# Optimization experiments

Measured on AMD Instinct MI355X. Metric: run time of the kernel, lower is better.

## Reference

```python
import jax, jax.numpy as jnp
import numpy as np

H = 128
N_ATOMS = 20000
N_BONDS = 60000
BATCH = 8


def _linear_params(key, fan_in, fan_out, bias=True):
    kw, kb = jax.random.split(key)
    lim = 1.0 / np.sqrt(fan_in)
    W = jax.random.uniform(kw, (fan_in, fan_out), jnp.float32, -lim, lim)
    if bias:
        b = jax.random.uniform(kb, (fan_out,), jnp.float32, -lim, lim)
        return W, b
    return W


def setup_inputs() -> dict:
    key = jax.random.key(0)
    ks = jax.random.split(key, 12)
    h = jax.random.normal(ks[0], (BATCH, N_ATOMS, H), jnp.float32)
    x = jax.random.normal(ks[1], (BATCH, N_ATOMS, 3), jnp.float32)
    bond_indices = jax.random.randint(ks[2], (N_BONDS, 2), 0, N_ATOMS, jnp.int64)
    Wm1, bm1 = _linear_params(ks[3], 2 * H + 1, H)
    Wm2, bm2 = _linear_params(ks[4], H, H)
    Wn1, bn1 = _linear_params(ks[5], 2 * H, H)
    Wn2, bn2 = _linear_params(ks[6], H, H)
    Wc1, bc1 = _linear_params(ks[7], H, H)
    # xavier_uniform gain=0.001 for final coord layer [1, H] in torch -> [H, 1] here
    lim = 0.001 * np.sqrt(6.0 / (H + 1))
    Wc2 = jax.random.uniform(ks[8], (H, 1), jnp.float32, -lim, lim)
    return dict(h=h, x=x, bond_indices=bond_indices,
                Wm1=Wm1, bm1=bm1, Wm2=Wm2, bm2=bm2,
                Wn1=Wn1, bn1=bn1, Wn2=Wn2, bn2=bn2,
                Wc1=Wc1, bc1=bc1, Wc2=Wc2)


def reference(h, x, bond_indices, Wm1, bm1, Wm2, bm2, Wn1, bn1, Wn2, bn2, Wc1, bc1, Wc2):
    silu = jax.nn.silu
    n_atoms = h.shape[1]
    src = bond_indices[:, 0]
    dst = bond_indices[:, 1]

    h_src = h[:, src, :]            # [B, E, H]
    h_dst = h[:, dst, :]
    coord_diff = x[:, dst, :] - x[:, src, :]   # [B, E, 3]
    dist = jnp.linalg.norm(coord_diff, axis=-1, keepdims=True)  # [B, E, 1]

    mi = jnp.concatenate([h_src, h_dst, dist], axis=-1)  # [B, E, 2H+1]
    messages = silu(silu(mi @ Wm1 + bm1) @ Wm2 + bm2)    # [B, E, H]

    aggregated = jnp.zeros_like(h).at[:, dst, :].add(messages).at[:, src, :].add(messages)

    h_in = jnp.concatenate([h, aggregated], axis=-1)     # [B, N, 2H]
    h_out = h + (silu(h_in @ Wn1 + bn1) @ Wn2 + bn2)

    coord_weights = silu(messages @ Wc1 + bc1) @ Wc2     # [B, E, 1]
    coord_diff_norm = coord_diff / (dist + 1e-8)
    upd = coord_diff_norm * coord_weights                # [B, E, 3]
    coord_update = jnp.zeros_like(x).at[:, dst, :].add(upd).at[:, src, :].add(-upd)

    ones = jnp.ones(src.shape[0], dtype=h.dtype)
    bond_counts = jnp.zeros(n_atoms, dtype=h.dtype).at[dst].add(ones).at[src].add(ones)
    bond_counts = jnp.clip(bond_counts, 1.0, None)
    x_out = x + coord_update / bond_counts[None, :, None]
    return h_out, x_out
```

## Files before the change

kernel.cpp:

```cpp
#include <hip/hip_runtime.h>


#define H      128
#define NA     20000
#define NB     60000
#define NBATCH 8
#define ADJ_CAP 32

typedef __bf16 bf16;
typedef __bf16 bf16x4 __attribute__((ext_vector_type(4)));
typedef __bf16 bf16x8 __attribute__((ext_vector_type(8)));
typedef float  f32x4  __attribute__((ext_vector_type(4)));

__device__ __forceinline__ float silu_f(float v) {
  float e = __expf(-v);
  return v * __builtin_amdgcn_rcpf(1.0f + e);
}

__device__ __forceinline__ int tswz(int row, int col) {
  return (row << 7) + (((((col) >> 3) ^ (row & 7)) << 3) | (col & 7));
}

__global__ void cast_h(const float* __restrict__ src, bf16* __restrict__ dst) {
  int i = blockIdx.x * 256 + threadIdx.x;
  float4 v = *(const float4*)(src + (size_t)i * 4);
  bf16x4 t = {(bf16)v.x, (bf16)v.y, (bf16)v.z, (bf16)v.w};
  *(bf16x4*)(dst + (size_t)i * 4) = t;
}

__device__ __forceinline__ void pack_one(const float* __restrict__ src,
                                         bf16* __restrict__ dst, int K,
                                         int i) {
  int k = i >> 7, n = i & 127;
  int nt = n >> 4, ks = k >> 5;
  int lane = (((k >> 3) & 3) << 4) | (n & 15);
  int j = k & 7;
  int KS = K >> 5;
  dst[((((nt * KS + ks) * 64) + lane) << 3) + j] = (bf16)src[i];
}

__global__ void pack_all(const float* __restrict__ Wm1,
                         const float* __restrict__ Wm2,
                         const float* __restrict__ Wn1,
                         const float* __restrict__ Wn2,
                         const float* __restrict__ Wc1,
                         bf16* __restrict__ W1p, bf16* __restrict__ W2p,
                         bf16* __restrict__ Wn1p, bf16* __restrict__ Wn2p,
                         bf16* __restrict__ Wc1p) {
  int i = blockIdx.x * 256 + threadIdx.x;
  if (i < 32768)       pack_one(Wm1, W1p, 256, i);
  else if (i < 49152)  pack_one(Wm2, W2p, 128, i - 32768);
  else if (i < 81920)  pack_one(Wn1, Wn1p, 256, i - 49152);
  else if (i < 98304)  pack_one(Wn2, Wn2p, 128, i - 81920);
  else if (i < 114688) pack_one(Wc1, Wc1p, 128, i - 98304);
}

__global__ void build_adj2(const int* __restrict__ bonds,
                           int* __restrict__ degI, int* __restrict__ adj2) {
  int e = blockIdx.x * 256 + threadIdx.x;
  if (e >= NB) return;
  int s = bonds[2 * e], d = bonds[2 * e + 1];
  int p = atomicAdd(&degI[s], 1);
  if (p < ADJ_CAP) adj2[s * ADJ_CAP + p] = (e << 1);
  p = atomicAdd(&degI[d], 1);
  if (p < ADJ_CAP) adj2[d * ADJ_CAP + p] = (e << 1) | 1;
}

__global__ __launch_bounds__(256, 4) void msg_kernel(
    const bf16* __restrict__ hb, const float* __restrict__ x,
    const int* __restrict__ bonds,
    const bf16* __restrict__ W1p, const float* __restrict__ bm1,
    const bf16* __restrict__ W2p, const float* __restrict__ bm2,
    const float* __restrict__ w1c,
    const bf16* __restrict__ Wc1p, const float* __restrict__ bc1,
    const float* __restrict__ Wc2,
    bf16* __restrict__ msgOut, float* __restrict__ updv) {
  __shared__ __align__(16) bf16 Tbuf[64 * 128];
  __shared__ __align__(16) float cds[64 * 3];
  __shared__ __align__(16) float dists[64];
  __shared__ __align__(16) float bm1s[128], bm2s[128], w1cs[128];
  __shared__ __align__(16) float bc1s[128], wc2s[128];
  __shared__ float cwpart[2][64];

  const int tid = threadIdx.x, blk = blockIdx.x;

  if (tid < 64) {
    int Rg = blk * 64 + tid;
    int bond = Rg >> 3, batch = Rg & 7;
    int s = bonds[2 * bond], dn = bonds[2 * bond + 1];
    const float* xs = x + (size_t)(batch * NA + s) * 3;
    const float* xd = x + (size_t)(batch * NA + dn) * 3;
    float c0 = xd[0] - xs[0], c1 = xd[1] - xs[1], c2 = xd[2] - xs[2];
    cds[tid * 3 + 0] = c0; cds[tid * 3 + 1] = c1; cds[tid * 3 + 2] = c2;
    dists[tid] = sqrtf(c0 * c0 + c1 * c1 + c2 * c2);
  }
  if (tid < 128) {
    bm1s[tid] = bm1[tid]; bm2s[tid] = bm2[tid]; w1cs[tid] = w1c[tid];
    bc1s[tid] = bc1[tid]; wc2s[tid] = Wc2[tid];
  }
  __syncthreads();

  const int lane = tid & 63;
  const int quad = lane >> 4, l16 = lane & 15;
  const int wave = tid >> 6;
  const int rowBase = (wave >> 1) * 32;
  const int colG = wave & 1;
  const int colBase = colG * 64;
  const bf16x8* W1v = (const bf16x8*)W1p;
  const bf16x8* W2v = (const bf16x8*)W2p;
  const bf16x8* Wc1v = (const bf16x8*)Wc1p;

  const int row0 = rowBase + l16, row1 = row0 + 16;
  const int Rg0 = blk * 64 + row0;
  const int bn0 = Rg0 >> 3, bat0 = Rg0 & 7;
  const bf16* hs0 = hb + (size_t)(bat0 * NA + bonds[2 * bn0]) * H;
  const bf16* hd0 = hb + (size_t)(bat0 * NA + bonds[2 * bn0 + 1]) * H;
  const int Rg1 = Rg0 + 16;
  const int bn1_ = Rg1 >> 3, bat1 = Rg1 & 7;
  const bf16* hs1 = hb + (size_t)(bat1 * NA + bonds[2 * bn1_]) * H;
  const bf16* hd1 = hb + (size_t)(bat1 * NA + bonds[2 * bn1_ + 1]) * H;
  const float dist0 = dists[row0], dist1 = dists[row1];

  f32x4 acc0[4], acc1[4];
#pragma unroll
  for (int nt = 0; nt < 4; nt++) {
    acc0[nt] = (f32x4){0.f, 0.f, 0.f, 0.f};
    acc1[nt] = (f32x4){0.f, 0.f, 0.f, 0.f};
  }

#pragma unroll
  for (int ks = 0; ks < 4; ks++) {
    bf16x8 a0 = *(const bf16x8*)(hs0 + ks * 32 + quad * 8);
    bf16x8 a1 = *(const bf16x8*)(hs1 + ks * 32 + quad * 8);
#pragma unroll
    for (int nt = 0; nt < 4; nt++) {
      bf16x8 b = W1v[((colG * 4 + nt) * 8 + ks) * 64 + lane];
      acc0[nt] = __builtin_amdgcn_mfma_f32_16x16x32_bf16(b, a0, acc0[nt], 0, 0, 0);
      acc1[nt] = __builtin_amdgcn_mfma_f32_16x16x32_bf16(b, a1, acc1[nt], 0, 0, 0);
    }
  }
#pragma unroll
  for (int ks = 4; ks < 8; ks++) {
    bf16x8 a0 = *(const bf16x8*)(hd0 + (ks - 4) * 32 + quad * 8);
    bf16x8 a1 = *(const bf16x8*)(hd1 + (ks - 4) * 32 + quad * 8);
#pragma unroll
    for (int nt = 0; nt < 4; nt++) {
      bf16x8 b = W1v[((colG * 4 + nt) * 8 + ks) * 64 + lane];
      acc0[nt] = __builtin_amdgcn_mfma_f32_16x16x32_bf16(b, a0, acc0[nt], 0, 0, 0);
      acc1[nt] = __builtin_amdgcn_mfma_f32_16x16x32_bf16(b, a1, acc1[nt], 0, 0, 0);
    }
  }
#pragma unroll
  for (int nt = 0; nt < 4; nt++) {
    int col = colBase + nt * 16 + quad * 4;
    f32x4 bb = *(const f32x4*)&bm1s[col];
    f32x4 wc = *(const f32x4*)&w1cs[col];
    bf16x4 o0, o1;
#pragma unroll
    for (int reg = 0; reg < 4; reg++) {
      o0[reg] = (bf16)silu_f(acc0[nt][reg] + bb[reg] + dist0 * wc[reg]);
      o1[reg] = (bf16)silu_f(acc1[nt][reg] + bb[reg] + dist1 * wc[reg]);
    }
    *(bf16x4*)&Tbuf[tswz(row0, col)] = o0;
    *(bf16x4*)&Tbuf[tswz(row1, col)] = o1;
  }
  __syncthreads();

#pragma unroll
  for (int nt = 0; nt < 4; nt++) {
    acc0[nt] = (f32x4){0.f, 0.f, 0.f, 0.f};
    acc1[nt] = (f32x4){0.f, 0.f, 0.f, 0.f};
  }
#pragma unroll
  for (int ks = 0; ks < 4; ks++) {
    bf16x8 a0 = *(const bf16x8*)&Tbuf[tswz(row0, ks * 32 + quad * 8)];
    bf16x8 a1 = *(const bf16x8*)&Tbuf[tswz(row1, ks * 32 + quad * 8)];
#pragma unroll
    for (int nt = 0; nt < 4; nt++) {
      bf16x8 b = W2v[((colG * 4 + nt) * 4 + ks) * 64 + lane];
      acc0[nt] = __builtin_amdgcn_mfma_f32_16x16x32_bf16(b, a0, acc0[nt], 0, 0, 0);
      acc1[nt] = __builtin_amdgcn_mfma_f32_16x16x32_bf16(b, a1, acc1[nt], 0, 0, 0);
    }
  }
  __syncthreads();
#pragma unroll
  for (int nt = 0; nt < 4; nt++) {
    int col = colBase + nt * 16 + quad * 4;
    f32x4 bb = *(const f32x4*)&bm2s[col];
    bf16x4 o0, o1;
#pragma unroll
    for (int reg = 0; reg < 4; reg++) {
      o0[reg] = (bf16)silu_f(acc0[nt][reg] + bb[reg]);
      o1[reg] = (bf16)silu_f(acc1[nt][reg] + bb[reg]);
    }
    *(bf16x4*)&Tbuf[tswz(row0, col)] = o0;
    *(bf16x4*)&Tbuf[tswz(row1, col)] = o1;
  }
  __syncthreads();

#pragma unroll
  for (int nt = 0; nt < 4; nt++) {
    acc0[nt] = (f32x4){0.f, 0.f, 0.f, 0.f};
    acc1[nt] = (f32x4){0.f, 0.f, 0.f, 0.f};
  }
#pragma unroll
  for (int ks = 0; ks < 4; ks++) {
    bf16x8 a0 = *(const bf16x8*)&Tbuf[tswz(row0, ks * 32 + quad * 8)];
    bf16x8 a1 = *(const bf16x8*)&Tbuf[tswz(row1, ks * 32 + quad * 8)];
#pragma unroll
    for (int nt = 0; nt < 4; nt++) {
      bf16x8 b = Wc1v[((colG * 4 + nt) * 4 + ks) * 64 + lane];
      acc0[nt] = __builtin_amdgcn_mfma_f32_16x16x32_bf16(b, a0, acc0[nt], 0, 0, 0);
      acc1[nt] = __builtin_amdgcn_mfma_f32_16x16x32_bf16(b, a1, acc1[nt], 0, 0, 0);
    }
  }

#pragma unroll
  for (int i = 0; i < 4; i++) {
    int item = i * 256 + tid;
    int row = item >> 4, cg = item & 15;
    *(bf16x8*)&msgOut[(size_t)(blk * 64 + row) * H + cg * 8] =
        *(const bf16x8*)&Tbuf[tswz(row, cg * 8)];
  }

  float s0 = 0.f, s1 = 0.f;
#pragma unroll
  for (int nt = 0; nt < 4; nt++) {
    int col = colBase + nt * 16 + quad * 4;
    f32x4 bb = *(const f32x4*)&bc1s[col];
    f32x4 w2 = *(const f32x4*)&wc2s[col];
#pragma unroll
    for (int reg = 0; reg < 4; reg++) {
      s0 += silu_f(acc0[nt][reg] + bb[reg]) * w2[reg];
      s1 += silu_f(acc1[nt][reg] + bb[reg]) * w2[reg];
    }
  }
  s0 += __shfl_xor(s0, 16); s0 += __shfl_xor(s0, 32);
  s1 += __shfl_xor(s1, 16); s1 += __shfl_xor(s1, 32);
  if (quad == 0) {
    cwpart[colG][row0] = s0;
    cwpart[colG][row1] = s1;
  }
  __syncthreads();
  if (colG == 0 && quad == 0) {
#pragma unroll
    for (int rs = 0; rs < 2; rs++) {
      int row = rs ? row1 : row0;
      size_t Rg = (size_t)blk * 64 + row;
      float cw = cwpart[0][row] + cwpart[1][row];
      float inv = 1.0f / (dists[row] + 1e-8f);
#pragma unroll
      for (int c = 0; c < 3; c++)
        updv[Rg * 3 + c] = cds[row * 3 + c] * inv * cw;
    }
  }
}

__global__ __launch_bounds__(256, 6) void node_kernel(
    const float* __restrict__ h, const bf16* __restrict__ hb,
    const bf16* __restrict__ msg, const float* __restrict__ updv,
    const int* __restrict__ degI, const int* __restrict__ adj2,
    const bf16* __restrict__ Wn1p, const float* __restrict__ bn1,
    const bf16* __restrict__ Wn2p, const float* __restrict__ bn2,
    const float* __restrict__ x,
    float* __restrict__ hout, float* __restrict__ xout) {
  __shared__ __align__(16) bf16 Abuf[32 * 128];
  __shared__ __align__(16) bf16 Tbuf[32 * 128];

  const int tid = threadIdx.x, blk = blockIdx.x;

  {
    const int row = tid >> 3, c8 = tid & 7;
    const int Rg = blk * 32 + row;
    const int atomA = Rg % NA, batA = Rg / NA;
    int deg = degI[atomA];
    if (deg > ADJ_CAP) deg = ADJ_CAP;
    const int* ap = adj2 + atomA * ADJ_CAP;
    float a16[16];
#pragma unroll
    for (int t = 0; t < 16; t++) a16[t] = 0.f;
    float sx = 0.f, sy = 0.f, sz = 0.f;
    int j = 0;
    for (; j + 4 <= deg; j += 4) {
      int4 e4 = *(const int4*)&ap[j];
      const bf16* m0 = msg + ((size_t)(e4.x >> 1) * 8 + batA) * H + c8 * 16;
      const bf16* m1 = msg + ((size_t)(e4.y >> 1) * 8 + batA) * H + c8 * 16;
      const bf16* m2 = msg + ((size_t)(e4.z >> 1) * 8 + batA) * H + c8 * 16;
      const bf16* m3 = msg + ((size_t)(e4.w >> 1) * 8 + batA) * H + c8 * 16;
      bf16x8 v0 = *(const bf16x8*)(m0), v1 = *(const bf16x8*)(m0 + 8);
      bf16x8 u0 = *(const bf16x8*)(m1), u1 = *(const bf16x8*)(m1 + 8);
      bf16x8 p0 = *(const bf16x8*)(m2), p1 = *(const bf16x8*)(m2 + 8);
      bf16x8 q0 = *(const bf16x8*)(m3), q1 = *(const bf16x8*)(m3 + 8);
      if (c8 == 0) {
        float sg0 = (e4.x & 1) ? 1.0f : -1.0f;
        float sg1 = (e4.y & 1) ? 1.0f : -1.0f;
        float sg2 = (e4.z & 1) ? 1.0f : -1.0f;
        float sg3 = (e4.w & 1) ? 1.0f : -1.0f;
        const float* uv0 = updv + ((size_t)(e4.x >> 1) * 8 + batA) * 3;
        const float* uv1 = updv + ((size_t)(e4.y >> 1) * 8 + batA) * 3;
        const float* uv2 = updv + ((size_t)(e4.z >> 1) * 8 + batA) * 3;
        const float* uv3 = updv + ((size_t)(e4.w >> 1) * 8 + batA) * 3;
        sx += sg0 * uv0[0] + sg1 * uv1[0] + sg2 * uv2[0] + sg3 * uv3[0];
        sy += sg0 * uv0[1] + sg1 * uv1[1] + sg2 * uv2[1] + sg3 * uv3[1];
        sz += sg0 * uv0[2] + sg1 * uv1[2] + sg2 * uv2[2] + sg3 * uv3[2];
      }
#pragma unroll
      for (int t = 0; t < 8; t++) {
        a16[t]     += ((float)v0[t] + (float)u0[t]) + ((float)p0[t] + (float)q0[t]);
        a16[8 + t] += ((float)v1[t] + (float)u1[t]) + ((float)p1[t] + (float)q1[t]);
      }
    }
    for (; j < deg; j++) {
      int ent0 = ap[j];
      const bf16* m0 = msg + ((size_t)(ent0 >> 1) * 8 + batA) * H + c8 * 16;
      bf16x8 v0 = *(const bf16x8*)(m0);
      bf16x8 v1 = *(const bf16x8*)(m0 + 8);
      if (c8 == 0) {
        float sg0 = (ent0 & 1) ? 1.0f : -1.0f;
        const float* uv0 = updv + ((size_t)(ent0 >> 1) * 8 + batA) * 3;
        sx += sg0 * uv0[0]; sy += sg0 * uv0[1]; sz += sg0 * uv0[2];
      }
#pragma unroll
      for (int t = 0; t < 8; t++) {
        a16[t]     += (float)v0[t];
        a16[8 + t] += (float)v1[t];
      }
    }
    if (c8 == 0) {
      float cnt = deg < 1 ? 1.0f : (float)deg;
      float inv = 1.0f / cnt;
      size_t o = (size_t)Rg * 3;
      xout[o + 0] = x[o + 0] + sx * inv;
      xout[o + 1] = x[o + 1] + sy * inv;
      xout[o + 2] = x[o + 2] + sz * inv;
    }
    bf16x8 w0, w1;
#pragma unroll
    for (int t = 0; t < 8; t++) { w0[t] = (bf16)a16[t]; w1[t] = (bf16)a16[8 + t]; }
    *(bf16x8*)&Abuf[tswz(row, c8 * 16)]     = w0;
    *(bf16x8*)&Abuf[tswz(row, c8 * 16 + 8)] = w1;
  }
  __syncthreads();

  const int lane = tid & 63, wave = tid >> 6;
  const int quad = lane >> 4, l16 = lane & 15;
  const int rowG = (wave >> 1) * 16, colG = wave & 1, colBase = colG * 64;
  const int rowL = rowG + l16;
  const size_t RgA = (size_t)blk * 32 + rowL;
  const bf16* hrow = hb + RgA * H;
  const bf16x8* W1v = (const bf16x8*)Wn1p;
  const bf16x8* W2v = (const bf16x8*)Wn2p;

  f32x4 acc[4];
#pragma unroll
  for (int nt = 0; nt < 4; nt++) acc[nt] = (f32x4){0.f, 0.f, 0.f, 0.f};

#pragma unroll
  for (int ks = 0; ks < 4; ks++) {
    bf16x8 a = *(const bf16x8*)(hrow + ks * 32 + quad * 8);
#pragma unroll
    for (int nt = 0; nt < 4; nt++) {
      bf16x8 b = W1v[((colG * 4 + nt) * 8 + ks) * 64 + lane];
      acc[nt] = __builtin_amdgcn_mfma_f32_16x16x32_bf16(b, a, acc[nt], 0, 0, 0);
    }
  }
#pragma unroll
  for (int ks2 = 0; ks2 < 4; ks2++) {
    bf16x8 a = *(const bf16x8*)&Abuf[tswz(rowL, ks2 * 32 + quad * 8)];
#pragma unroll
    for (int nt = 0; nt < 4; nt++) {
      bf16x8 b = W1v[((colG * 4 + nt) * 8 + 4 + ks2) * 64 + lane];
      acc[nt] = __builtin_amdgcn_mfma_f32_16x16x32_bf16(b, a, acc[nt], 0, 0, 0);
    }
  }
#pragma unroll
  for (int nt = 0; nt < 4; nt++) {
    int col = colBase + nt * 16 + quad * 4;
    f32x4 bb = *(const f32x4*)&bn1[col];
    bf16x4 o;
#pragma unroll
    for (int reg = 0; reg < 4; reg++)
      o[reg] = (bf16)silu_f(acc[nt][reg] + bb[reg]);
    *(bf16x4*)&Tbuf[tswz(rowL, col)] = o;
  }
  __syncthreads();

#pragma unroll
  for (int nt = 0; nt < 4; nt++) acc[nt] = (f32x4){0.f, 0.f, 0.f, 0.f};
#pragma unroll
  for (int ks = 0; ks < 4; ks++) {
    bf16x8 a = *(const bf16x8*)&Tbuf[tswz(rowL, ks * 32 + quad * 8)];
#pragma unroll
    for (int nt = 0; nt < 4; nt++) {
      bf16x8 b = W2v[((colG * 4 + nt) * 4 + ks) * 64 + lane];
      acc[nt] = __builtin_amdgcn_mfma_f32_16x16x32_bf16(b, a, acc[nt], 0, 0, 0);
    }
  }
#pragma unroll
  for (int nt = 0; nt < 4; nt++) {
    int col = colBase + nt * 16 + quad * 4;
    f32x4 bb = *(const f32x4*)&bn2[col];
    f32x4 hv = *(const f32x4*)&h[RgA * H + col];
    f32x4 o;
#pragma unroll
    for (int reg = 0; reg < 4; reg++)
      o[reg] = hv[reg] + acc[nt][reg] + bb[reg];
    *(f32x4*)&hout[RgA * H + col] = o;
  }
}

extern "C" void kernel_launch(void* const* d_in, const int* in_sizes, int n_in,
                              void* d_out, int out_size, void* d_ws,
                              size_t ws_size, hipStream_t stream) {
  const float* h    = (const float*)d_in[0];
  const float* x    = (const float*)d_in[1];
  const int*  bonds = (const int*)d_in[2];
  const float* Wm1  = (const float*)d_in[3];
  const float* bm1  = (const float*)d_in[4];
  const float* Wm2  = (const float*)d_in[5];
  const float* bm2  = (const float*)d_in[6];
  const float* Wn1  = (const float*)d_in[7];
  const float* bn1  = (const float*)d_in[8];
  const float* Wn2  = (const float*)d_in[9];
  const float* bn2  = (const float*)d_in[10];
  const float* Wc1  = (const float*)d_in[11];
  const float* bc1  = (const float*)d_in[12];
  const float* Wc2  = (const float*)d_in[13];

  float* out  = (float*)d_out;
  float* hout = out;
  float* xout = out + (size_t)NBATCH * NA * H;

  char* ws = (char*)d_ws;
  const size_t OFF_DEG  = 0;
  const size_t OFF_W1   = 163840;
  const size_t OFF_W2   = OFF_W1 + 65536;
  const size_t OFF_WN1  = OFF_W2 + 32768;
  const size_t OFF_WN2  = OFF_WN1 + 65536;
  const size_t OFF_WC1  = OFF_WN2 + 32768;
  const size_t OFF_ADJ2 = 393216;
  const size_t OFF_UPDV = 2953216;
  const size_t OFF_HB   = 8713216;
  const size_t OFF_MSG  = 49673216;

  int*   degI = (int*)(ws + OFF_DEG);
  bf16*  W1p  = (bf16*)(ws + OFF_W1);
  bf16*  W2p  = (bf16*)(ws + OFF_W2);
  bf16*  Wn1p = (bf16*)(ws + OFF_WN1);
  bf16*  Wn2p = (bf16*)(ws + OFF_WN2);
  bf16*  Wc1p = (bf16*)(ws + OFF_WC1);
  int*   adj2 = (int*)(ws + OFF_ADJ2);
  float* updv = (float*)(ws + OFF_UPDV);
  bf16*  hb   = (bf16*)(ws + OFF_HB);
  bf16*  msgB = (bf16*)(ws + OFF_MSG);

  (void)hipMemsetAsync(degI, 0, NA * sizeof(int), stream);

  cast_h<<<NBATCH * NA * H / 1024, 256, 0, stream>>>(h, hb);
  pack_all<<<448, 256, 0, stream>>>(Wm1, Wm2, Wn1, Wn2, Wc1,
                                    W1p, W2p, Wn1p, Wn2p, Wc1p);
  build_adj2<<<(NB + 255) / 256, 256, 0, stream>>>(bonds, degI, adj2);

  msg_kernel<<<NB * NBATCH / 64, 256, 0, stream>>>(
      hb, x, bonds, W1p, bm1, W2p, bm2, Wm1 + 256 * H, Wc1p, bc1, Wc2,
      msgB, updv);
  node_kernel<<<NBATCH * NA / 32, 256, 0, stream>>>(
      h, hb, msgB, updv, degI, adj2, Wn1p, bn1, Wn2p, bn2, x,
      hout, xout);
}
```

Baseline: 447.0 us.

## Double node-kernel row tile to 64 so each weight fragment feeds two MFMAs

The node kernel now handles 64 atom rows per block instead of 32. Each wave computes two 16-row MFMA tiles that share every loaded weight fragment, which halves the global weight traffic per row. The gather phase now gives each thread 32 columns with 2-way edge unrolling instead of 16 columns with 4-way. The cost is more registers and shared memory per block (launch bounds drop from 6 to 4 blocks per CU) and half as many blocks in the grid.

```diff
diff --git a/kernel.cpp b/kernel.cpp
--- a/kernel.cpp
+++ b/kernel.cpp
@@ -256,7 +256,7 @@
   }
 }
 
-__global__ __launch_bounds__(256, 6) void node_kernel(
+__global__ __launch_bounds__(256, 4) void node_kernel(
     const float* __restrict__ h, const bf16* __restrict__ hb,
     const bf16* __restrict__ msg, const float* __restrict__ updv,
     const int* __restrict__ degI, const int* __restrict__ adj2,
@@ -264,69 +264,64 @@
     const bf16* __restrict__ Wn2p, const float* __restrict__ bn2,
     const float* __restrict__ x,
     float* __restrict__ hout, float* __restrict__ xout) {
-  __shared__ __align__(16) bf16 Abuf[32 * 128];
-  __shared__ __align__(16) bf16 Tbuf[32 * 128];
+  __shared__ __align__(16) bf16 Abuf[64 * 128];
+  __shared__ __align__(16) bf16 Tbuf[64 * 128];
 
   const int tid = threadIdx.x, blk = blockIdx.x;
 
   {
-    const int row = tid >> 3, c8 = tid & 7;
-    const int Rg = blk * 32 + row;
+    const int row = tid >> 2, c4 = tid & 3;
+    const int Rg = blk * 64 + row;
     const int atomA = Rg % NA, batA = Rg / NA;
     int deg = degI[atomA];
     if (deg > ADJ_CAP) deg = ADJ_CAP;
     const int* ap = adj2 + atomA * ADJ_CAP;
-    float a16[16];
-#pragma unroll
-    for (int t = 0; t < 16; t++) a16[t] = 0.f;
+    float a32[32];
+#pragma unroll
+    for (int t = 0; t < 32; t++) a32[t] = 0.f;
     float sx = 0.f, sy = 0.f, sz = 0.f;
     int j = 0;
-    for (; j + 4 <= deg; j += 4) {
-      int4 e4 = *(const int4*)&ap[j];
-      const bf16* m0 = msg + ((size_t)(e4.x >> 1) * 8 + batA) * H + c8 * 16;
-      const bf16* m1 = msg + ((size_t)(e4.y >> 1) * 8 + batA) * H + c8 * 16;
-      const bf16* m2 = msg + ((size_t)(e4.z >> 1) * 8 + batA) * H + c8 * 16;
-      const bf16* m3 = msg + ((size_t)(e4.w >> 1) * 8 + batA) * H + c8 * 16;
-      bf16x8 v0 = *(const bf16x8*)(m0), v1 = *(const bf16x8*)(m0 + 8);
-      bf16x8 u0 = *(const bf16x8*)(m1), u1 = *(const bf16x8*)(m1 + 8);
-      bf16x8 p0 = *(const bf16x8*)(m2), p1 = *(const bf16x8*)(m2 + 8);
-      bf16x8 q0 = *(const bf16x8*)(m3), q1 = *(const bf16x8*)(m3 + 8);
-      if (c8 == 0) {
-        float sg0 = (e4.x & 1) ? 1.0f : -1.0f;
-        float sg1 = (e4.y & 1) ? 1.0f : -1.0f;
-        float sg2 = (e4.z & 1) ? 1.0f : -1.0f;
-        float sg3 = (e4.w & 1) ? 1.0f : -1.0f;
-        const float* uv0 = updv + ((size_t)(e4.x >> 1) * 8 + batA) * 3;
-        const float* uv1 = updv + ((size_t)(e4.y >> 1) * 8 + batA) * 3;
-        const float* uv2 = updv + ((size_t)(e4.z >> 1) * 8 + batA) * 3;
-        const float* uv3 = updv + ((size_t)(e4.w >> 1) * 8 + batA) * 3;
-        sx += sg0 * uv0[0] + sg1 * uv1[0] + sg2 * uv2[0] + sg3 * uv3[0];
-        sy += sg0 * uv0[1] + sg1 * uv1[1] + sg2 * uv2[1] + sg3 * uv3[1];
-        sz += sg0 * uv0[2] + sg1 * uv1[2] + sg2 * uv2[2] + sg3 * uv3[2];
+    for (; j + 2 <= deg; j += 2) {
+      int2 e2 = *(const int2*)&ap[j];
+      const bf16* m0 = msg + ((size_t)(e2.x >> 1) * 8 + batA) * H + c4 * 32;
+      const bf16* m1 = msg + ((size_t)(e2.y >> 1) * 8 + batA) * H + c4 * 32;
+      bf16x8 v0 = *(const bf16x8*)(m0),      v1 = *(const bf16x8*)(m0 + 8);
+      bf16x8 v2 = *(const bf16x8*)(m0 + 16), v3 = *(const bf16x8*)(m0 + 24);
+      bf16x8 u0 = *(const bf16x8*)(m1),      u1 = *(const bf16x8*)(m1 + 8);
+      bf16x8 u2 = *(const bf16x8*)(m1 + 16), u3 = *(const bf16x8*)(m1 + 24);
+      if (c4 == 0) {
+        float sg0 = (e2.x & 1) ? 1.0f : -1.0f;
+        float sg1 = (e2.y & 1) ? 1.0f : -1.0f;
+        const float* uv0 = updv + ((size_t)(e2.x >> 1) * 8 + batA) * 3;
+        const float* uv1 = updv + ((size_t)(e2.y >> 1) * 8 + batA) * 3;
+        sx += sg0 * uv0[0] + sg1 * uv1[0];
+        sy += sg0 * uv0[1] + sg1 * uv1[1];
+        sz += sg0 * uv0[2] + sg1 * uv1[2];
       }
 #pragma unroll
       for (int t = 0; t < 8; t++) {
-        a16[t]     += ((float)v0[t] + (float)u0[t]) + ((float)p0[t] + (float)q0[t]);
-        a16[8 + t] += ((float)v1[t] + (float)u1[t]) + ((float)p1[t] + (float)q1[t]);
+        a32[t]      += (float)v0[t] + (float)u0[t];
+        a32[8 + t]  += (float)v1[t] + (float)u1[t];
+        a32[16 + t] += (float)v2[t] + (float)u2[t];
+        a32[24 + t] += (float)v3[t] + (float)u3[t];
       }
     }
-    for (; j < deg; j++) {
+    if (j < deg) {
       int ent0 = ap[j];
-      const bf16* m0 = msg + ((size_t)(ent0 >> 1) * 8 + batA) * H + c8 * 16;
-      bf16x8 v0 = *(const bf16x8*)(m0);
-      bf16x8 v1 = *(const bf16x8*)(m0 + 8);
-      if (c8 == 0) {
+      const bf16* m0 = msg + ((size_t)(ent0 >> 1) * 8 + batA) * H + c4 * 32;
+      if (c4 == 0) {
         float sg0 = (ent0 & 1) ? 1.0f : -1.0f;
         const float* uv0 = updv + ((size_t)(ent0 >> 1) * 8 + batA) * 3;
         sx += sg0 * uv0[0]; sy += sg0 * uv0[1]; sz += sg0 * uv0[2];
       }
 #pragma unroll
-      for (int t = 0; t < 8; t++) {
-        a16[t]     += (float)v0[t];
-        a16[8 + t] += (float)v1[t];
+      for (int k = 0; k < 4; k++) {
+        bf16x8 v = *(const bf16x8*)(m0 + 8 * k);
+#pragma unroll
+        for (int t = 0; t < 8; t++) a32[8 * k + t] += (float)v[t];
       }
     }
-    if (c8 == 0) {
+    if (c4 == 0) {
       float cnt = deg < 1 ? 1.0f : (float)deg;
       float inv = 1.0f / cnt;
       size_t o = (size_t)Rg * 3;
@@ -334,78 +329,101 @@
       xout[o + 1] = x[o + 1] + sy * inv;
       xout[o + 2] = x[o + 2] + sz * inv;
     }
-    bf16x8 w0, w1;
-#pragma unroll
-    for (int t = 0; t < 8; t++) { w0[t] = (bf16)a16[t]; w1[t] = (bf16)a16[8 + t]; }
-    *(bf16x8*)&Abuf[tswz(row, c8 * 16)]     = w0;
-    *(bf16x8*)&Abuf[tswz(row, c8 * 16 + 8)] = w1;
+#pragma unroll
+    for (int k = 0; k < 4; k++) {
+      bf16x8 w;
+#pragma unroll
+      for (int t = 0; t < 8; t++) w[t] = (bf16)a32[8 * k + t];
+      *(bf16x8*)&Abuf[tswz(row, c4 * 32 + 8 * k)] = w;
+    }
   }
   __syncthreads();
 
   const int lane = tid & 63, wave = tid >> 6;
   const int quad = lane >> 4, l16 = lane & 15;
-  const int rowG = (wave >> 1) * 16, colG = wave & 1, colBase = colG * 64;
-  const int rowL = rowG + l16;
-  const size_t RgA = (size_t)blk * 32 + rowL;
-  const bf16* hrow = hb + RgA * H;
+  const int rowBase = (wave >> 1) * 32, colG = wave & 1, colBase = colG * 64;
+  const int row0 = rowBase + l16, row1 = row0 + 16;
+  const size_t RgA0 = (size_t)blk * 64 + row0;
+  const size_t RgA1 = RgA0 + 16;
+  const bf16* hrow0 = hb + RgA0 * H;
+  const bf16* hrow1 = hb + RgA1 * H;
   const bf16x8* W1v = (const bf16x8*)Wn1p;
   const bf16x8* W2v = (const bf16x8*)Wn2p;
 
-  f32x4 acc[4];
-#pragma unroll
-  for (int nt = 0; nt < 4; nt++) acc[nt] = (f32x4){0.f, 0.f, 0.f, 0.f};
+  f32x4 acc0[4], acc1[4];
+#pragma unroll
+  for (int nt = 0; nt < 4; nt++) {
+    acc0[nt] = (f32x4){0.f, 0.f, 0.f, 0.f};
+    acc1[nt] = (f32x4){0.f, 0.f, 0.f, 0.f};
+  }
 
 #pragma unroll
   for (int ks = 0; ks < 4; ks++) {
-    bf16x8 a = *(const bf16x8*)(hrow + ks * 32 + quad * 8);
+    bf16x8 a0 = *(const bf16x8*)(hrow0 + ks * 32 + quad * 8);
+    bf16x8 a1 = *(const bf16x8*)(hrow1 + ks * 32 + quad * 8);
 #pragma unroll
     for (int nt = 0; nt < 4; nt++) {
       bf16x8 b = W1v[((colG * 4 + nt) * 8 + ks) * 64 + lane];
-      acc[nt] = __builtin_amdgcn_mfma_f32_16x16x32_bf16(b, a, acc[nt], 0, 0, 0);
+      acc0[nt] = __builtin_amdgcn_mfma_f32_16x16x32_bf16(b, a0, acc0[nt], 0, 0, 0);
+      acc1[nt] = __builtin_amdgcn_mfma_f32_16x16x32_bf16(b, a1, acc1[nt], 0, 0, 0);
     }
   }
 #pragma unroll
   for (int ks2 = 0; ks2 < 4; ks2++) {
-    bf16x8 a = *(const bf16x8*)&Abuf[tswz(rowL, ks2 * 32 + quad * 8)];
+    bf16x8 a0 = *(const bf16x8*)&Abuf[tswz(row0, ks2 * 32 + quad * 8)];
+    bf16x8 a1 = *(const bf16x8*)&Abuf[tswz(row1, ks2 * 32 + quad * 8)];
 #pragma unroll
     for (int nt = 0; nt < 4; nt++) {
       bf16x8 b = W1v[((colG * 4 + nt) * 8 + 4 + ks2) * 64 + lane];
-      acc[nt] = __builtin_amdgcn_mfma_f32_16x16x32_bf16(b, a, acc[nt], 0, 0, 0);
+      acc0[nt] = __builtin_amdgcn_mfma_f32_16x16x32_bf16(b, a0, acc0[nt], 0, 0, 0);
+      acc1[nt] = __builtin_amdgcn_mfma_f32_16x16x32_bf16(b, a1, acc1[nt], 0, 0, 0);
     }
   }
 #pragma unroll
   for (int nt = 0; nt < 4; nt++) {
     int col = colBase + nt * 16 + quad * 4;
     f32x4 bb = *(const f32x4*)&bn1[col];
-    bf16x4 o;
-#pragma unroll
-    for (int reg = 0; reg < 4; reg++)
-      o[reg] = (bf16)silu_f(acc[nt][reg] + bb[reg]);
-    *(bf16x4*)&Tbuf[tswz(rowL, col)] = o;
-  }
-  __syncthreads();
-
-#pragma unroll
-  for (int nt = 0; nt < 4; nt++) acc[nt] = (f32x4){0.f, 0.f, 0.f, 0.f};
+    bf16x4 o0, o1;
+#pragma unroll
+    for (int reg = 0; reg < 4; reg++) {
+      o0[reg] = (bf16)silu_f(acc0[nt][reg] + bb[reg]);
+      o1[reg] = (bf16)silu_f(acc1[nt][reg] + bb[reg]);
+    }
+    *(bf16x4*)&Tbuf[tswz(row0, col)] = o0;
+    *(bf16x4*)&Tbuf[tswz(row1, col)] = o1;
+  }
+  __syncthreads();
+
+#pragma unroll
+  for (int nt = 0; nt < 4; nt++) {
+    acc0[nt] = (f32x4){0.f, 0.f, 0.f, 0.f};
+    acc1[nt] = (f32x4){0.f, 0.f, 0.f, 0.f};
+  }
 #pragma unroll
   for (int ks = 0; ks < 4; ks++) {
-    bf16x8 a = *(const bf16x8*)&Tbuf[tswz(rowL, ks * 32 + quad * 8)];
+    bf16x8 a0 = *(const bf16x8*)&Tbuf[tswz(row0, ks * 32 + quad * 8)];
+    bf16x8 a1 = *(const bf16x8*)&Tbuf[tswz(row1, ks * 32 + quad * 8)];
 #pragma unroll
     for (int nt = 0; nt < 4; nt++) {
       bf16x8 b = W2v[((colG * 4 + nt) * 4 + ks) * 64 + lane];
-      acc[nt] = __builtin_amdgcn_mfma_f32_16x16x32_bf16(b, a, acc[nt], 0, 0, 0);
+      acc0[nt] = __builtin_amdgcn_mfma_f32_16x16x32_bf16(b, a0, acc0[nt], 0, 0, 0);
+      acc1[nt] = __builtin_amdgcn_mfma_f32_16x16x32_bf16(b, a1, acc1[nt], 0, 0, 0);
     }
   }
 #pragma unroll
   for (int nt = 0; nt < 4; nt++) {
     int col = colBase + nt * 16 + quad * 4;
     f32x4 bb = *(const f32x4*)&bn2[col];
-    f32x4 hv = *(const f32x4*)&h[RgA * H + col];
-    f32x4 o;
-#pragma unroll
-    for (int reg = 0; reg < 4; reg++)
-      o[reg] = hv[reg] + acc[nt][reg] + bb[reg];
-    *(f32x4*)&hout[RgA * H + col] = o;
+    f32x4 hv0 = *(const f32x4*)&h[RgA0 * H + col];
+    f32x4 hv1 = *(const f32x4*)&h[RgA1 * H + col];
+    f32x4 o0, o1;
+#pragma unroll
+    for (int reg = 0; reg < 4; reg++) {
+      o0[reg] = hv0[reg] + acc0[nt][reg] + bb[reg];
+      o1[reg] = hv1[reg] + acc1[nt][reg] + bb[reg];
+    }
+    *(f32x4*)&hout[RgA0 * H + col] = o0;
+    *(f32x4*)&hout[RgA1 * H + col] = o1;
   }
 }
 
@@ -464,7 +482,7 @@
   msg_kernel<<<NB * NBATCH / 64, 256, 0, stream>>>(
       hb, x, bonds, W1p, bm1, W2p, bm2, Wm1 + 256 * H, Wc1p, bc1, Wc2,
       msgB, updv);
-  node_kernel<<<NBATCH * NA / 32, 256, 0, stream>>>(
+  node_kernel<<<NBATCH * NA / 64, 256, 0, stream>>>(
       h, hb, msgB, updv, degI, adj2, Wn1p, bn1, Wn2p, bn2, x,
       hout, xout);
 }
```

Measured after the change: 433.0 us. 1.03x faster.
